# Kernel optimization log

Hardware: AMD Instinct MI355X
Metric: run time of the kernel (lower is better)

## Reference

```python
import jax, jax.numpy as jnp
import numpy as np

S, B, C = 7, 2, 20
L_COORD, L_NOOBJ = 5.0, 0.5
BATCH = 16384


def setup_inputs() -> dict:
    key = jax.random.key(0)
    k1, k2, k3 = jax.random.split(key, 3)
    pred = jax.random.normal(k1, (BATCH, S, S, 5 * B + C), dtype=jnp.float32)
    target = jax.random.uniform(k2, (BATCH, S, S, 5 * B + C), dtype=jnp.float32)
    conf = target[..., 4]
    target = target.at[..., 4].set(jnp.where(conf > 0.9, conf, 0.0))
    # per-cell branch choice (replaces python random.random() > 0.5 per object)
    choice = jax.random.randint(k3, (BATCH, S, S), 0, 2, dtype=jnp.int32)
    return {"pred": pred, "target": target, "choice": choice}


def reference(pred, target, choice):
    dt = pred.dtype
    tconf = target[..., 4]
    obj = tconf > 0                      # [B,S,S]
    m = obj.astype(dt)
    n_obj = jnp.maximum(m.sum(), 1.0)
    c = choice.astype(bool)              # True -> box 1, False -> box 2
    cE = c[..., None]

    pxy = jnp.where(cE, pred[..., 0:2], pred[..., 5:7])
    pwh = jnp.where(cE, pred[..., 2:4], pred[..., 7:9])
    txy = jnp.where(cE, target[..., 0:2], target[..., 5:7])
    twh = jnp.where(cE, target[..., 2:4], target[..., 7:9])
    twh = jnp.where(obj[..., None], twh, 1.0)  # sqrt-safe outside obj mask
    pobj = jnp.where(c, pred[..., 4], pred[..., 9])
    tobj = jnp.where(c, tconf, target[..., 9])

    # per-object: mean over 2 elems for xy and for (wh - sqrt(twh)), summed over objects
    loc_cell = ((pxy - txy) ** 2).mean(-1) + ((pwh - jnp.sqrt(twh)) ** 2).mean(-1)
    loc_loss = L_COORD * (m * loc_cell).sum()
    obj_loss = (m * (pobj - tobj) ** 2).sum()

    nm = (tconf == 0).astype(dt)
    n_no = jnp.maximum(nm.sum(), 1.0)
    noobj_loss = L_NOOBJ * (
        (nm * (pred[..., 4] - tconf) ** 2).sum() / n_no
        + (nm * (pred[..., 9] - target[..., 9]) ** 2).sum() / n_no
    )

    # faithful to original: softmax applied BEFORE CrossEntropyLoss (double softmax)
    logits = pred[..., 5 * B:5 * B + C]
    sm = jax.nn.softmax(logits, axis=-1)
    logp = jax.nn.log_softmax(sm, axis=-1)
    tcls = jnp.argmax(target[..., 5 * B:5 * B + C], axis=-1)
    ce = -jnp.take_along_axis(logp, tcls[..., None], axis=-1)[..., 0]
    cls_loss = (m * ce).sum() / n_obj

    return (loc_loss, cls_loss, obj_loss, noobj_loss)
```

## Files before the change

### kernel.cpp

```cpp
#include <hip/hip_runtime.h>
#include <math.h>


constexpr int NCH = 30;
constexpr int CC  = 20;
constexpr int ROW = 8;
constexpr int T   = 128;
constexpr int CPB = 128;
constexpr int NV  = CPB * NCH / 4;

__global__ __launch_bounds__(T) void yolo_main(
    const float* __restrict__ pred, const float* __restrict__ target,
    const int* __restrict__ choice, float* __restrict__ ws, int ncells)
{
    __shared__ float sbuf[2 * CPB * NCH];
    const int tid = threadIdx.x;
    const long long cell0 = (long long)blockIdx.x * CPB;
    const int remain = ncells - (int)cell0;

    if (remain >= CPB) {
        const float4* Pg = (const float4*)(pred + cell0 * NCH);
        const float4* Tg = (const float4*)(target + cell0 * NCH);
        #pragma unroll
        for (int j = 0; j < 2 * NV / T; ++j) {
            int k = j * T + tid;
            float4 v;
            if (k < NV) v = Pg[k]; else v = Tg[k - NV];
            *(float4*)&sbuf[k * 4] = v;
        }
    } else {
        int nf = remain * NCH;
        for (int idx = tid; idx < nf; idx += T) {
            sbuf[idx]             = pred[cell0 * NCH + idx];
            sbuf[CPB * NCH + idx] = target[cell0 * NCH + idx];
        }
    }
    __syncthreads();

    float s_loc = 0.f, s_ce = 0.f, s_obj = 0.f, s_no = 0.f;
    float n_obj = 0.f, n_no = 0.f;

    if (cell0 + tid < ncells) {
        const float* sp  = &sbuf[tid * NCH];
        const float* stt = &sbuf[CPB * NCH + tid * NCH];
        float p[NCH], t[NCH];
        #pragma unroll
        for (int i = 0; i < NCH / 2; ++i) {
            float2 v = *(const float2*)&sp[2 * i];  p[2*i] = v.x; p[2*i+1] = v.y;
        }
        #pragma unroll
        for (int i = 0; i < NCH / 2; ++i) {
            float2 w = *(const float2*)&stt[2 * i]; t[2*i] = w.x; t[2*i+1] = w.y;
        }
        bool c = choice[cell0 + tid] != 0;

        float tconf = t[4];
        bool  obj = tconf > 0.0f;
        float m = obj ? 1.0f : 0.0f;

        float pxy0 = c ? p[0] : p[5];
        float pxy1 = c ? p[1] : p[6];
        float pwh0 = c ? p[2] : p[7];
        float pwh1 = c ? p[3] : p[8];
        float pobj = c ? p[4] : p[9];
        float txy0 = c ? t[0] : t[5];
        float txy1 = c ? t[1] : t[6];
        float twh0 = c ? t[2] : t[7];
        float twh1 = c ? t[3] : t[8];
        if (!obj) { twh0 = 1.0f; twh1 = 1.0f; }
        float tobj = c ? tconf : t[9];

        float dx = pxy0 - txy0, dy = pxy1 - txy1;
        float dw = pwh0 - sqrtf(twh0), dh = pwh1 - sqrtf(twh1);
        s_loc = m * (0.5f * (dx * dx + dy * dy) + 0.5f * (dw * dw + dh * dh));

        float dob = pobj - tobj;
        s_obj = m * dob * dob;

        float nm = (tconf == 0.0f) ? 1.0f : 0.0f;
        float d4 = p[4] - tconf, d9 = p[9] - t[9];
        s_no = nm * (d4 * d4 + d9 * d9);

        n_obj = m;
        n_no  = nm;

        int   tcls  = 0;
        float tbest = t[10];
        #pragma unroll
        for (int i = 1; i < CC; ++i) {
            float v = t[10 + i];
            if (v > tbest) { tbest = v; tcls = i; }
        }
        float mx = p[10];
        #pragma unroll
        for (int i = 1; i < CC; ++i) mx = fmaxf(mx, p[10 + i]);
        float e[CC];
        float Z = 0.f;
        #pragma unroll
        for (int i = 0; i < CC; ++i) { e[i] = __expf(p[10 + i] - mx); Z += e[i]; }
        float rZ = 1.0f / Z;
        float Z2 = 0.f, sm_t = 0.f;
        #pragma unroll
        for (int i = 0; i < CC; ++i) {
            float sm = e[i] * rZ;
            Z2 += __expf(sm);
            if (i == tcls) sm_t = sm;
        }
        s_ce = m * (__logf(Z2) - sm_t);
    }

    #pragma unroll
    for (int off = 32; off > 0; off >>= 1) {
        s_loc += __shfl_down(s_loc, off);
        s_ce  += __shfl_down(s_ce,  off);
        s_obj += __shfl_down(s_obj, off);
        s_no  += __shfl_down(s_no,  off);
        n_obj += __shfl_down(n_obj, off);
        n_no  += __shfl_down(n_no,  off);
    }

    __shared__ float red[2][6];
    int wave = tid >> 6;
    int lane = tid & 63;
    if (lane == 0) {
        red[wave][0] = s_loc; red[wave][1] = s_ce;  red[wave][2] = s_obj;
        red[wave][3] = s_no;  red[wave][4] = n_obj; red[wave][5] = n_no;
    }
    __syncthreads();
    if (tid < 6) {
        float v = red[0][tid] + red[1][tid];
        ws[(size_t)blockIdx.x * ROW + tid] = v;
    }
}

__global__ __launch_bounds__(256) void yolo_reduce(
    const float* __restrict__ ws, float* __restrict__ out, int nb)
{
    float s[6] = {0.f, 0.f, 0.f, 0.f, 0.f, 0.f};
    for (int b = threadIdx.x; b < nb; b += 256) {
        #pragma unroll
        for (int j = 0; j < 6; ++j) s[j] += ws[(size_t)b * ROW + j];
    }
    #pragma unroll
    for (int off = 32; off > 0; off >>= 1) {
        #pragma unroll
        for (int j = 0; j < 6; ++j) s[j] += __shfl_down(s[j], off);
    }
    __shared__ float red[4][6];
    int wave = threadIdx.x >> 6;
    int lane = threadIdx.x & 63;
    if (lane == 0) {
        #pragma unroll
        for (int j = 0; j < 6; ++j) red[wave][j] = s[j];
    }
    __syncthreads();
    if (threadIdx.x == 0) {
        float t[6];
        #pragma unroll
        for (int j = 0; j < 6; ++j)
            t[j] = red[0][j] + red[1][j] + red[2][j] + red[3][j];
        out[0] = 5.0f * t[0];
        out[1] = t[1] / fmaxf(t[4], 1.0f);
        out[2] = t[2];
        out[3] = 0.5f * t[3] / fmaxf(t[5], 1.0f);
    }
}

extern "C" void kernel_launch(void* const* d_in, const int* in_sizes, int n_in,
                              void* d_out, int out_size, void* d_ws, size_t ws_size,
                              hipStream_t stream) {
    const float* pred   = (const float*)d_in[0];
    const float* target = (const float*)d_in[1];
    const int*   choice = (const int*)d_in[2];
    float* out = (float*)d_out;
    float* ws  = (float*)d_ws;

    int ncells = in_sizes[2];
    int blocks = (ncells + CPB - 1) / CPB;
    yolo_main<<<blocks, T, 0, stream>>>(pred, target, choice, ws, ncells);
    yolo_reduce<<<1, 256, 0, stream>>>(ws, out, blocks);
}
```

Measured before the change: 214.3 us.

## Make main kernel persistent and prefetch the next chunk into registers

Replaces the one-block-per-128-cells launch with a fixed grid of 1280 persistent blocks of 256 threads that loop over cell chunks. While the current chunk is computed from shared memory, the next chunk's pred/target float4s and choice values are already loaded into registers, so global load latency overlaps with the softmax/loss arithmetic. Per-thread accumulators carry across chunks, and the final reduce reads fewer partial rows. The cost is higher register pressure, and only half the threads do the per-cell compute.

```diff
diff --git a/kernel.cpp b/kernel.cpp
--- a/kernel.cpp
+++ b/kernel.cpp
@@ -5,130 +5,171 @@
 constexpr int NCH = 30;
 constexpr int CC  = 20;
 constexpr int ROW = 8;
-constexpr int T   = 128;
+constexpr int T   = 256;
 constexpr int CPB = 128;
-constexpr int NV  = CPB * NCH / 4;
+constexpr int NF4 = CPB * NCH * 2 / 4;
+constexpr int HF4 = NF4 / 2;
+constexpr int GRID = 1280;
+
+__device__ __forceinline__ void issue_chunk(
+    const float* __restrict__ pred, const float* __restrict__ target,
+    const int* __restrict__ choice, int cc, int ncells, int tid,
+    float4 (&r)[8], int& ci)
+{
+    long long base = (long long)cc * CPB;
+    if (base + CPB <= (long long)ncells) {
+        const float4* Pb = (const float4*)(pred + base * NCH);
+        const float4* Tb = (const float4*)(target + base * NCH);
+        #pragma unroll
+        for (int j = 0; j < 8; ++j) {
+            int k = j * T + tid;
+            if (k < NF4) r[j] = (k < HF4) ? Pb[k] : Tb[k - HF4];
+        }
+    } else {
+        int nfl = (int)(ncells - base) * NCH;
+        const float* Pf = pred + base * NCH;
+        const float* Tf = target + base * NCH;
+        #pragma unroll
+        for (int j = 0; j < 8; ++j) {
+            int k = j * T + tid;
+            float4 v = make_float4(0.f, 0.f, 0.f, 0.f);
+            if (k < NF4) {
+                int kk = (k < HF4) ? k : k - HF4;
+                const float* src = (k < HF4) ? Pf : Tf;
+                int b = 4 * kk;
+                if (b + 0 < nfl) v.x = src[b + 0];
+                if (b + 1 < nfl) v.y = src[b + 1];
+                if (b + 2 < nfl) v.z = src[b + 2];
+                if (b + 3 < nfl) v.w = src[b + 3];
+            }
+            r[j] = v;
+        }
+    }
+    if (tid < CPB) {
+        long long ce = base + tid;
+        ci = (ce < (long long)ncells) ? choice[ce] : 0;
+    }
+}
 
 __global__ __launch_bounds__(T) void yolo_main(
     const float* __restrict__ pred, const float* __restrict__ target,
-    const int* __restrict__ choice, float* __restrict__ ws, int ncells)
+    const int* __restrict__ choice, float* __restrict__ ws,
+    int ncells, int nchunks)
 {
     __shared__ float sbuf[2 * CPB * NCH];
     const int tid = threadIdx.x;
-    const long long cell0 = (long long)blockIdx.x * CPB;
-    const int remain = ncells - (int)cell0;
-
-    if (remain >= CPB) {
-        const float4* Pg = (const float4*)(pred + cell0 * NCH);
-        const float4* Tg = (const float4*)(target + cell0 * NCH);
-        #pragma unroll
-        for (int j = 0; j < 2 * NV / T; ++j) {
+
+    float a_loc = 0.f, a_ce = 0.f, a_obj = 0.f, a_no = 0.f;
+    float a_nob = 0.f, a_nno = 0.f;
+
+    float4 r[8];
+    int ci = 0;
+    int c = blockIdx.x;
+    if (c < nchunks) issue_chunk(pred, target, choice, c, ncells, tid, r, ci);
+
+    for (; c < nchunks; c += GRID) {
+        __syncthreads();
+        #pragma unroll
+        for (int j = 0; j < 8; ++j) {
             int k = j * T + tid;
-            float4 v;
-            if (k < NV) v = Pg[k]; else v = Tg[k - NV];
-            *(float4*)&sbuf[k * 4] = v;
-        }
-    } else {
-        int nf = remain * NCH;
-        for (int idx = tid; idx < nf; idx += T) {
-            sbuf[idx]             = pred[cell0 * NCH + idx];
-            sbuf[CPB * NCH + idx] = target[cell0 * NCH + idx];
-        }
-    }
-    __syncthreads();
-
-    float s_loc = 0.f, s_ce = 0.f, s_obj = 0.f, s_no = 0.f;
-    float n_obj = 0.f, n_no = 0.f;
-
-    if (cell0 + tid < ncells) {
-        const float* sp  = &sbuf[tid * NCH];
-        const float* stt = &sbuf[CPB * NCH + tid * NCH];
-        float p[NCH], t[NCH];
-        #pragma unroll
-        for (int i = 0; i < NCH / 2; ++i) {
-            float2 v = *(const float2*)&sp[2 * i];  p[2*i] = v.x; p[2*i+1] = v.y;
-        }
-        #pragma unroll
-        for (int i = 0; i < NCH / 2; ++i) {
-            float2 w = *(const float2*)&stt[2 * i]; t[2*i] = w.x; t[2*i+1] = w.y;
-        }
-        bool c = choice[cell0 + tid] != 0;
-
-        float tconf = t[4];
-        bool  obj = tconf > 0.0f;
-        float m = obj ? 1.0f : 0.0f;
-
-        float pxy0 = c ? p[0] : p[5];
-        float pxy1 = c ? p[1] : p[6];
-        float pwh0 = c ? p[2] : p[7];
-        float pwh1 = c ? p[3] : p[8];
-        float pobj = c ? p[4] : p[9];
-        float txy0 = c ? t[0] : t[5];
-        float txy1 = c ? t[1] : t[6];
-        float twh0 = c ? t[2] : t[7];
-        float twh1 = c ? t[3] : t[8];
-        if (!obj) { twh0 = 1.0f; twh1 = 1.0f; }
-        float tobj = c ? tconf : t[9];
-
-        float dx = pxy0 - txy0, dy = pxy1 - txy1;
-        float dw = pwh0 - sqrtf(twh0), dh = pwh1 - sqrtf(twh1);
-        s_loc = m * (0.5f * (dx * dx + dy * dy) + 0.5f * (dw * dw + dh * dh));
-
-        float dob = pobj - tobj;
-        s_obj = m * dob * dob;
-
-        float nm = (tconf == 0.0f) ? 1.0f : 0.0f;
-        float d4 = p[4] - tconf, d9 = p[9] - t[9];
-        s_no = nm * (d4 * d4 + d9 * d9);
-
-        n_obj = m;
-        n_no  = nm;
-
-        int   tcls  = 0;
-        float tbest = t[10];
-        #pragma unroll
-        for (int i = 1; i < CC; ++i) {
-            float v = t[10 + i];
-            if (v > tbest) { tbest = v; tcls = i; }
-        }
-        float mx = p[10];
-        #pragma unroll
-        for (int i = 1; i < CC; ++i) mx = fmaxf(mx, p[10 + i]);
-        float e[CC];
-        float Z = 0.f;
-        #pragma unroll
-        for (int i = 0; i < CC; ++i) { e[i] = __expf(p[10 + i] - mx); Z += e[i]; }
-        float rZ = 1.0f / Z;
-        float Z2 = 0.f, sm_t = 0.f;
-        #pragma unroll
-        for (int i = 0; i < CC; ++i) {
-            float sm = e[i] * rZ;
-            Z2 += __expf(sm);
-            if (i == tcls) sm_t = sm;
-        }
-        s_ce = m * (__logf(Z2) - sm_t);
+            if (k < NF4) *(float4*)&sbuf[k * 4] = r[j];
+        }
+        int myc = ci;
+        __syncthreads();
+
+        int cn = c + GRID;
+        if (cn < nchunks) issue_chunk(pred, target, choice, cn, ncells, tid, r, ci);
+
+        if (tid < CPB && (long long)c * CPB + tid < ncells) {
+            const float* sp  = &sbuf[tid * NCH];
+            const float* stt = &sbuf[CPB * NCH + tid * NCH];
+            float p[NCH], t[NCH];
+            #pragma unroll
+            for (int i = 0; i < NCH / 2; ++i) {
+                float2 v = *(const float2*)&sp[2 * i];  p[2*i] = v.x; p[2*i+1] = v.y;
+            }
+            #pragma unroll
+            for (int i = 0; i < NCH / 2; ++i) {
+                float2 w = *(const float2*)&stt[2 * i]; t[2*i] = w.x; t[2*i+1] = w.y;
+            }
+            bool csel = myc != 0;
+
+            float tconf = t[4];
+            bool  obj = tconf > 0.0f;
+            float m = obj ? 1.0f : 0.0f;
+
+            float pxy0 = csel ? p[0] : p[5];
+            float pxy1 = csel ? p[1] : p[6];
+            float pwh0 = csel ? p[2] : p[7];
+            float pwh1 = csel ? p[3] : p[8];
+            float pobj = csel ? p[4] : p[9];
+            float txy0 = csel ? t[0] : t[5];
+            float txy1 = csel ? t[1] : t[6];
+            float twh0 = csel ? t[2] : t[7];
+            float twh1 = csel ? t[3] : t[8];
+            if (!obj) { twh0 = 1.0f; twh1 = 1.0f; }
+            float tobj = csel ? tconf : t[9];
+
+            float dx = pxy0 - txy0, dy = pxy1 - txy1;
+            float dw = pwh0 - sqrtf(twh0), dh = pwh1 - sqrtf(twh1);
+            a_loc += m * (0.5f * (dx*dx + dy*dy) + 0.5f * (dw*dw + dh*dh));
+
+            float dob = pobj - tobj;
+            a_obj += m * dob * dob;
+
+            float nm = (tconf == 0.0f) ? 1.0f : 0.0f;
+            float d4 = p[4] - tconf, d9 = p[9] - t[9];
+            a_no += nm * (d4 * d4 + d9 * d9);
+
+            a_nob += m;
+            a_nno += nm;
+
+            int   tcls  = 0;
+            float tbest = t[10];
+            #pragma unroll
+            for (int i = 1; i < CC; ++i) {
+                float v = t[10 + i];
+                if (v > tbest) { tbest = v; tcls = i; }
+            }
+            float mx = p[10];
+            #pragma unroll
+            for (int i = 1; i < CC; ++i) mx = fmaxf(mx, p[10 + i]);
+            float e[CC];
+            float Z = 0.f;
+            #pragma unroll
+            for (int i = 0; i < CC; ++i) { e[i] = __expf(p[10+i] - mx); Z += e[i]; }
+            float rZ = 1.0f / Z;
+            float Z2 = 0.f, sm_t = 0.f;
+            #pragma unroll
+            for (int i = 0; i < CC; ++i) {
+                float sm = e[i] * rZ;
+                Z2 += __expf(sm);
+                if (i == tcls) sm_t = sm;
+            }
+            a_ce += m * (__logf(Z2) - sm_t);
+        }
     }
 
     #pragma unroll
     for (int off = 32; off > 0; off >>= 1) {
-        s_loc += __shfl_down(s_loc, off);
-        s_ce  += __shfl_down(s_ce,  off);
-        s_obj += __shfl_down(s_obj, off);
-        s_no  += __shfl_down(s_no,  off);
-        n_obj += __shfl_down(n_obj, off);
-        n_no  += __shfl_down(n_no,  off);
-    }
-
-    __shared__ float red[2][6];
+        a_loc += __shfl_down(a_loc, off);
+        a_ce  += __shfl_down(a_ce,  off);
+        a_obj += __shfl_down(a_obj, off);
+        a_no  += __shfl_down(a_no,  off);
+        a_nob += __shfl_down(a_nob, off);
+        a_nno += __shfl_down(a_nno, off);
+    }
+
+    __shared__ float red[4][6];
     int wave = tid >> 6;
     int lane = tid & 63;
     if (lane == 0) {
-        red[wave][0] = s_loc; red[wave][1] = s_ce;  red[wave][2] = s_obj;
-        red[wave][3] = s_no;  red[wave][4] = n_obj; red[wave][5] = n_no;
+        red[wave][0] = a_loc; red[wave][1] = a_ce;  red[wave][2] = a_obj;
+        red[wave][3] = a_no;  red[wave][4] = a_nob; red[wave][5] = a_nno;
     }
     __syncthreads();
     if (tid < 6) {
-        float v = red[0][tid] + red[1][tid];
+        float v = red[0][tid] + red[1][tid] + red[2][tid] + red[3][tid];
         ws[(size_t)blockIdx.x * ROW + tid] = v;
     }
 }
@@ -175,8 +216,9 @@
     float* out = (float*)d_out;
     float* ws  = (float*)d_ws;
 
-    int ncells = in_sizes[2];
-    int blocks = (ncells + CPB - 1) / CPB;
-    yolo_main<<<blocks, T, 0, stream>>>(pred, target, choice, ws, ncells);
-    yolo_reduce<<<1, 256, 0, stream>>>(ws, out, blocks);
-}
+    int ncells  = in_sizes[2];
+    int nchunks = (ncells + CPB - 1) / CPB;
+    int grid    = GRID < nchunks ? GRID : nchunks;
+    yolo_main<<<grid, T, 0, stream>>>(pred, target, choice, ws, ncells, nchunks);
+    yolo_reduce<<<1, 256, 0, stream>>>(ws, out, grid);
+}
```

After: 211.4 us. Within noise of the previous version (-1.4%).
